# Kernel optimization log

Hardware: AMD Instinct MI355X
Metric: run time of the kernel (lower is better)

The kernel has to match this reference:

```python
import jax, jax.numpy as jnp
import numpy as np
from jax import lax

S, D_IN, D_FC, H_LSTM, H_RNN, D_OUT = 16384, 6, 20, 48, 24, 2


def _lstm_layer(seq, Wih, Whh, bih, bhh):
    # seq: [S, d_in]; PyTorch gate order: i, f, g, o
    H = Whh.shape[1]
    xW = seq @ Wih.T + (bih + bhh)  # [S, 4H] precomputed input projections

    def step(carry, xw):
        h, c = carry
        g = xw + h @ Whh.T
        i = jax.nn.sigmoid(g[:H])
        f = jax.nn.sigmoid(g[H:2 * H])
        gg = jnp.tanh(g[2 * H:3 * H])
        o = jax.nn.sigmoid(g[3 * H:])
        c = f * c + i * gg
        h = o * jnp.tanh(c)
        return (h, c), h

    z = jnp.zeros((H,), seq.dtype)
    _, hs = lax.scan(step, (z, z), xW)
    return hs  # [S, H]


def _rnn_layer(seq, Wih, Whh, bih, bhh):
    H = Whh.shape[1]
    xW = seq @ Wih.T + (bih + bhh)

    def step(h, xw):
        h = jnp.tanh(xw + h @ Whh.T)
        return h, h

    _, hs = lax.scan(step, jnp.zeros((H,), seq.dtype), xW)
    return hs


def setup_inputs() -> dict:
    key = jax.random.key(0)
    ks = iter(jax.random.split(key, 32))

    def p(shape, fan_in):
        s = 1.0 / np.sqrt(fan_in)
        return jax.random.uniform(next(ks), shape, jnp.float32, -s, s)

    inp = {"x": jax.random.normal(next(ks), (S, D_IN), jnp.float32)}
    inp["fc1_W"] = p((D_FC, D_IN), D_IN)
    inp["fc1_b"] = p((D_FC,), D_IN)
    inp["fc2_W"] = p((D_FC, D_FC), D_FC)
    inp["fc2_b"] = p((D_FC,), D_FC)
    # LSTM layer 0: input 20 -> hidden 48
    inp["lstm0_Wih"] = p((4 * H_LSTM, D_FC), H_LSTM)
    inp["lstm0_Whh"] = p((4 * H_LSTM, H_LSTM), H_LSTM)
    inp["lstm0_bih"] = p((4 * H_LSTM,), H_LSTM)
    inp["lstm0_bhh"] = p((4 * H_LSTM,), H_LSTM)
    # LSTM layers 1..4: input 48 -> hidden 48, stacked
    inp["lstmr_Wih"] = p((4, 4 * H_LSTM, H_LSTM), H_LSTM)
    inp["lstmr_Whh"] = p((4, 4 * H_LSTM, H_LSTM), H_LSTM)
    inp["lstmr_bih"] = p((4, 4 * H_LSTM), H_LSTM)
    inp["lstmr_bhh"] = p((4, 4 * H_LSTM), H_LSTM)
    # RNN layer 0: 48 -> 24, layer 1: 24 -> 24
    inp["rnn0_Wih"] = p((H_RNN, H_LSTM), H_RNN)
    inp["rnn0_Whh"] = p((H_RNN, H_RNN), H_RNN)
    inp["rnn0_bih"] = p((H_RNN,), H_RNN)
    inp["rnn0_bhh"] = p((H_RNN,), H_RNN)
    inp["rnn1_Wih"] = p((H_RNN, H_RNN), H_RNN)
    inp["rnn1_Whh"] = p((H_RNN, H_RNN), H_RNN)
    inp["rnn1_bih"] = p((H_RNN,), H_RNN)
    inp["rnn1_bhh"] = p((H_RNN,), H_RNN)
    inp["fc4_W"] = p((D_OUT, H_RNN), H_RNN)
    inp["fc4_b"] = p((D_OUT,), H_RNN)
    return inp


def reference(x, fc1_W, fc1_b, fc2_W, fc2_b,
              lstm0_Wih, lstm0_Whh, lstm0_bih, lstm0_bhh,
              lstmr_Wih, lstmr_Whh, lstmr_bih, lstmr_bhh,
              rnn0_Wih, rnn0_Whh, rnn0_bih, rnn0_bhh,
              rnn1_Wih, rnn1_Whh, rnn1_bih, rnn1_bhh,
              fc4_W, fc4_b):
    h = jax.nn.relu(x @ fc1_W.T + fc1_b)
    h = jax.nn.relu(h @ fc2_W.T + fc2_b)
    h = _lstm_layer(h, lstm0_Wih, lstm0_Whh, lstm0_bih, lstm0_bhh)
    for l in range(4):  # fixed small layer loop
        h = _lstm_layer(h, lstmr_Wih[l], lstmr_Whh[l], lstmr_bih[l], lstmr_bhh[l])
    h = _rnn_layer(h, rnn0_Wih, rnn0_Whh, rnn0_bih, rnn0_bhh)
    h = _rnn_layer(h, rnn1_Wih, rnn1_Whh, rnn1_bih, rnn1_bhh)
    h = jax.nn.relu(h)
    out = h @ fc4_W.T + fc4_b  # [S, 2]
    return out[None]  # [1, S, 2] matching batch_first torch output
```

## Files before the change

kernel.cpp:

```cpp
#include <hip/hip_runtime.h>
#include <hip/hip_bf16.h>

#define S_LEN 16384
#define N_IN 23
#define CH2 32
#define NCH2 (S_LEN / CH2)
#define RING_D 8

typedef float v2f __attribute__((ext_vector_type(2)));
typedef _Float16 h2v __attribute__((ext_vector_type(2)));

__device__ __forceinline__ float fsig(float x) {
    return __builtin_amdgcn_rcpf(1.f + __expf(-x));
}
__device__ __forceinline__ float ftanh_fast(float x) {
    float e = __expf(-2.f * fabsf(x));
    float r = (1.f - e) * __builtin_amdgcn_rcpf(1.f + e);
    return x >= 0.f ? r : -r;
}
__device__ __forceinline__ float rlane(float v, int k) {
    return __uint_as_float(__builtin_amdgcn_readlane(__float_as_uint(v), k));
}
__device__ __forceinline__ h2v rlane_h2(h2v v, int k) {
    int b;
    __builtin_memcpy(&b, &v, 4);
    b = __builtin_amdgcn_readlane(b, k);
    h2v r;
    __builtin_memcpy(&r, &b, 4);
    return r;
}
__device__ __forceinline__ h2v pack_h2(float a, float b) {
    auto p = __builtin_amdgcn_cvt_pkrtz(a, b);
    h2v r;
    __builtin_memcpy(&r, &p, 4);
    return r;
}

#if __has_builtin(__builtin_amdgcn_fdot2)
__device__ __forceinline__ float fdot2_hw(h2v w, h2v h, float acc) {
    return __builtin_amdgcn_fdot2(w, h, acc, false);
}
#define FDOT2(w, h, acc) fdot2_hw((w), (h), (acc))
#else
__device__ __forceinline__ float fdot2_sw(h2v w, h2v h, float acc) {
    return acc + (float)w.x * (float)h.x + (float)w.y * (float)h.y;
}
#define FDOT2(w, h, acc) fdot2_sw((w), (h), (acc))
#endif

__global__ void detect_kernel(const void* probe, int nsamp, int* flag)
{
    if (blockIdx.x == 0 && threadIdx.x == 0) {
        const unsigned short* p = (const unsigned short*)probe;
        int isbf16 = 1;
        for (int i = 0; i < nsamp; i++) {
            float v = __uint_as_float(((unsigned int)p[i]) << 16);
            if (!(fabsf(v) < 1e4f)) { isbf16 = 0; break; }
        }
        *flag = isbf16;
    }
}

struct IngestArgs {
    const void* src[N_IN];
    float*      dst[N_IN];
    int         n[N_IN];
};

__global__ void ingest_kernel(IngestArgs args, const int* __restrict__ flag)
{
    const int isbf16 = *flag;
    const int tid    = blockIdx.x * blockDim.x + threadIdx.x;
    const int stride = gridDim.x * blockDim.x;
    for (int i = 0; i < N_IN; i++) {
        const int n = args.n[i];
        float* dst  = args.dst[i];
        if (isbf16) {
            const unsigned short* s = (const unsigned short*)args.src[i];
            for (int j = tid; j < n; j += stride)
                dst[j] = __uint_as_float(((unsigned int)s[j]) << 16);
        } else {
            const float* s = (const float*)args.src[i];
            for (int j = tid; j < n; j += stride)
                dst[j] = s[j];
        }
    }
}

__global__ void init_kernel(int* prog)
{
    int t = threadIdx.x;
    if (t < 1024) prog[t] = 0;
}

__global__ void fc12_kernel(const float* __restrict__ x,
                            const float* __restrict__ W1, const float* __restrict__ b1,
                            const float* __restrict__ W2, const float* __restrict__ b2,
                            float* __restrict__ h2out)
{
    int s = blockIdx.x * blockDim.x + threadIdx.x;
    if (s >= S_LEN) return;
    float xin[6];
#pragma unroll
    for (int k = 0; k < 6; k++) xin[k] = x[s * 6 + k];
    float h1[20];
#pragma unroll
    for (int j = 0; j < 20; j++) {
        float a = b1[j];
#pragma unroll
        for (int k = 0; k < 6; k++) a += W1[j * 6 + k] * xin[k];
        h1[j] = a > 0.f ? a : 0.f;
    }
#pragma unroll
    for (int j = 0; j < 20; j++) {
        float a = b2[j];
#pragma unroll
        for (int k = 0; k < 20; k++) a += W2[j * 20 + k] * h1[k];
        h2out[s * 20 + j] = a > 0.f ? a : 0.f;
    }
}

template <int DIN, int NG, bool TRANS>
__device__ void producer_block(const float* __restrict__ in,
                               const float* __restrict__ Wih,
                               const float* __restrict__ bih,
                               const float* __restrict__ bhh,
                               float* __restrict__ ring,
                               int* my_prog, int* in_prog, int* cons_prog,
                               float* smem)
{
    constexpr int GR  = NG / 3;
    constexpr int GS  = 256 / GR;
    constexpr int SLT = CH2 / GS;

    const int t  = threadIdx.x;
    const int rg = t % GR;
    const int sg = t / GR;

    float* in_sh = smem;
    float* xw_sh = smem + CH2 * DIN;

    float w[3][DIN];
    float bs[3];
    int cellr[3], partr[3];
#pragma unroll
    for (int r = 0; r < 3; r++) {
        const int row = rg * 3 + r;
#pragma unroll
        for (int k = 0; k < DIN; k++) w[r][k] = Wih[row * DIN + k];
        bs[r] = bih[row] + bhh[row];
        cellr[r] = row % 48;
        partr[r] = row / 48;
    }

    const float4* x4 = (const float4*)in_sh;

    for (int c = 0; c < NCH2; c++) {
        if (t == 0) {
            if (in_prog) {
                while (__hip_atomic_load(in_prog, __ATOMIC_ACQUIRE, __HIP_MEMORY_SCOPE_AGENT) < c + 1)
                    __builtin_amdgcn_s_sleep(1);
            }
            if (c >= RING_D) {
                while (__hip_atomic_load(cons_prog, __ATOMIC_ACQUIRE, __HIP_MEMORY_SCOPE_AGENT) < c - RING_D + 1)
                    __builtin_amdgcn_s_sleep(1);
            }
        }
        __syncthreads();
        {
            const float4* gsrc = (const float4*)(in + (size_t)c * CH2 * DIN);
            float4* ldst = (float4*)in_sh;
            for (int i = t; i < CH2 * DIN / 4; i += 256) ldst[i] = gsrc[i];
        }
        __syncthreads();

#pragma unroll
        for (int i = 0; i < SLT; i++) {
            const int sl = sg * SLT + i;
            float a0 = bs[0], a1 = bs[1], a2 = bs[2];
#pragma unroll
            for (int k = 0; k < DIN / 4; k++) {
                float4 xv = x4[sl * (DIN / 4) + k];
                a0 += w[0][4 * k + 0] * xv.x; a0 += w[0][4 * k + 1] * xv.y;
                a0 += w[0][4 * k + 2] * xv.z; a0 += w[0][4 * k + 3] * xv.w;
                a1 += w[1][4 * k + 0] * xv.x; a1 += w[1][4 * k + 1] * xv.y;
                a1 += w[1][4 * k + 2] * xv.z; a1 += w[1][4 * k + 3] * xv.w;
                a2 += w[2][4 * k + 0] * xv.x; a2 += w[2][4 * k + 1] * xv.y;
                a2 += w[2][4 * k + 2] * xv.z; a2 += w[2][4 * k + 3] * xv.w;
            }
            if (TRANS) {
                xw_sh[(sl * 48 + cellr[0]) * 4 + partr[0]] = a0;
                xw_sh[(sl * 48 + cellr[1]) * 4 + partr[1]] = a1;
                xw_sh[(sl * 48 + cellr[2]) * 4 + partr[2]] = a2;
            } else {
                xw_sh[sl * NG + rg * 3 + 0] = a0;
                xw_sh[sl * NG + rg * 3 + 1] = a1;
                xw_sh[sl * NG + rg * 3 + 2] = a2;
            }
        }
        __syncthreads();
        {
            const float4* lsrc = (const float4*)xw_sh;
            float4* gdst = (float4*)(ring + (size_t)(c % RING_D) * CH2 * NG);
            for (int i = t; i < CH2 * NG / 4; i += 256) gdst[i] = lsrc[i];
        }
        __syncthreads();
        if (t == 0)
            __hip_atomic_store(my_prog, c + 1, __ATOMIC_RELEASE, __HIP_MEMORY_SCOPE_AGENT);
    }
}

__device__ void lstm_scan(const float* __restrict__ Whh,
                          const float* __restrict__ ring,
                          float* __restrict__ hseq,
                          int* my_prog, int* prod_prog, float* smem)
{
    const int t = threadIdx.x;
    const int j = (t < 48) ? t : 47;
    float* xw_buf = smem;
    float* hh_buf = smem + 12288;

    h2v wI[24], wF[24], wG[24], wO[24];
    if (t < 64) {
#pragma unroll
        for (int k = 0; k < 24; k++) {
            wI[k] = pack_h2(Whh[j * 48 + 2 * k],         Whh[j * 48 + 2 * k + 1]);
            wF[k] = pack_h2(Whh[(48 + j) * 48 + 2 * k],  Whh[(48 + j) * 48 + 2 * k + 1]);
            wG[k] = pack_h2(Whh[(96 + j) * 48 + 2 * k],  Whh[(96 + j) * 48 + 2 * k + 1]);
            wO[k] = pack_h2(Whh[(144 + j) * 48 + 2 * k], Whh[(144 + j) * 48 + 2 * k + 1]);
        }
    }
    float hvec = 0.f, ccell = 0.f;

    if (t >= 128) {
        while (__hip_atomic_load(prod_prog, __ATOMIC_ACQUIRE, __HIP_MEMORY_SCOPE_AGENT) < 1)
            __builtin_amdgcn_s_sleep(8);
        const float4* g = (const float4*)ring;
        float4* d = (float4*)xw_buf;
        for (int i = t - 128; i < CH2 * 48; i += 128) d[i] = g[i];
    }
    __syncthreads();

    for (int c = 0; c < NCH2; c++) {
        if (t < 64) {
            const float4* xf = (const float4*)(xw_buf + (c & 1) * (CH2 * 192));
            float* hh = hh_buf + (c & 1) * (CH2 * 48);
            float4 xw4 = xf[j];
            for (int sl = 0; sl < CH2; sl++) {
                float4 nxt = xf[(sl + 1 < CH2 ? sl + 1 : sl) * 48 + j];
                float hn = __shfl_down(hvec, 1, 64);
                h2v hp = pack_h2(hvec, hn);
                float aI0 = xw4.x, aF0 = xw4.y, aG0 = xw4.z, aO0 = xw4.w;
                float aI1 = 0.f, aF1 = 0.f, aG1 = 0.f, aO1 = 0.f;
#pragma unroll
                for (int kp = 0; kp < 12; kp++) {
                    h2v hb = rlane_h2(hp, 2 * kp);
                    aI0 = FDOT2(wI[kp], hb, aI0);
                    aF0 = FDOT2(wF[kp], hb, aF0);
                    aG0 = FDOT2(wG[kp], hb, aG0);
                    aO0 = FDOT2(wO[kp], hb, aO0);
                }
#pragma unroll
                for (int kp = 12; kp < 24; kp++) {
                    h2v hb = rlane_h2(hp, 2 * kp);
                    aI1 = FDOT2(wI[kp], hb, aI1);
                    aF1 = FDOT2(wF[kp], hb, aF1);
                    aG1 = FDOT2(wG[kp], hb, aG1);
                    aO1 = FDOT2(wO[kp], hb, aO1);
                }
                float iv = fsig(aI0 + aI1);
                float fv = fsig(aF0 + aF1);
                float gv = 2.f * fsig(2.f * (aG0 + aG1)) - 1.f;
                float ov = fsig(aO0 + aO1);
                ccell = fv * ccell + iv * gv;
                float h = ov * ftanh_fast(ccell);
                hvec = h;
                if (t < 48) hh[sl * 48 + t] = h;
                xw4 = nxt;
            }
        } else if (t < 128) {
            if (c >= 1) {
                const float4* s4 = (const float4*)(hh_buf + ((c - 1) & 1) * (CH2 * 48));
                float4* d4 = (float4*)(hseq + (size_t)(c - 1) * CH2 * 48);
                for (int i = t - 64; i < CH2 * 12; i += 64) d4[i] = s4[i];
                if (t == 64)
                    __hip_atomic_store(my_prog, c, __ATOMIC_RELEASE, __HIP_MEMORY_SCOPE_AGENT);
            }
        } else {
            if (c + 1 < NCH2) {
                while (__hip_atomic_load(prod_prog, __ATOMIC_ACQUIRE, __HIP_MEMORY_SCOPE_AGENT) < c + 2)
                    __builtin_amdgcn_s_sleep(8);
                const float4* g = (const float4*)(ring + (size_t)((c + 1) % RING_D) * CH2 * 192);
                float4* d = (float4*)(xw_buf + ((c + 1) & 1) * (CH2 * 192));
                for (int i = t - 128; i < CH2 * 48; i += 128) d[i] = g[i];
            }
        }
        __syncthreads();
    }
    if (t >= 64 && t < 128) {
        const float4* s4 = (const float4*)(hh_buf + ((NCH2 - 1) & 1) * (CH2 * 48));
        float4* d4 = (float4*)(hseq + (size_t)(NCH2 - 1) * CH2 * 48);
        for (int i = t - 64; i < CH2 * 12; i += 64) d4[i] = s4[i];
        if (t == 64)
            __hip_atomic_store(my_prog, NCH2, __ATOMIC_RELEASE, __HIP_MEMORY_SCOPE_AGENT);
    }
}

__device__ void rnn_scan(const float* __restrict__ Whh,
                         const float* __restrict__ ring,
                         float* __restrict__ hseq,
                         int* my_prog, int* prod_prog, float* smem)
{
    const int t = threadIdx.x;
    float* xw_buf = smem;
    float* hh_buf = smem + 1536;

    float whh[24];
    if (t < 24) {
#pragma unroll
        for (int k = 0; k < 24; k++) whh[k] = Whh[t * 24 + k];
    }
    float hvec = 0.f;

    if (t >= 128) {
        while (__hip_atomic_load(prod_prog, __ATOMIC_ACQUIRE, __HIP_MEMORY_SCOPE_AGENT) < 1)
            __builtin_amdgcn_s_sleep(8);
        const float4* g = (const float4*)ring;
        float4* d = (float4*)xw_buf;
        for (int i = t - 128; i < CH2 * 6; i += 128) d[i] = g[i];
    }
    __syncthreads();

    for (int c = 0; c < NCH2; c++) {
        if (t < 64) {
            const float* xwc = xw_buf + (c & 1) * (CH2 * 24);
            float* hh = hh_buf + (c & 1) * (CH2 * 24);
            float xwv = (t < 24) ? xwc[t] : 0.f;
            for (int sl = 0; sl < CH2; sl++) {
                float nxtx = (t < 24) ? xwc[((sl + 1 < CH2) ? sl + 1 : sl) * 24 + t] : 0.f;
                float a0 = xwv, a1 = 0.f, a2 = 0.f, a3 = 0.f;
#pragma unroll
                for (int k = 0; k < 24; k += 4) {
                    a0 += rlane(hvec, k + 0) * whh[k + 0];
                    a1 += rlane(hvec, k + 1) * whh[k + 1];
                    a2 += rlane(hvec, k + 2) * whh[k + 2];
                    a3 += rlane(hvec, k + 3) * whh[k + 3];
                }
                float h = ftanh_fast((a0 + a1) + (a2 + a3));
                if (t < 24) {
                    hvec = h;
                    hh[sl * 24 + t] = h;
                }
                xwv = nxtx;
            }
        } else if (t < 128) {
            if (c >= 1) {
                const float4* s4 = (const float4*)(hh_buf + ((c - 1) & 1) * (CH2 * 24));
                float4* d4 = (float4*)(hseq + (size_t)(c - 1) * CH2 * 24);
                for (int i = t - 64; i < CH2 * 6; i += 64) d4[i] = s4[i];
                if (t == 64)
                    __hip_atomic_store(my_prog, c, __ATOMIC_RELEASE, __HIP_MEMORY_SCOPE_AGENT);
            }
        } else {
            if (c + 1 < NCH2) {
                while (__hip_atomic_load(prod_prog, __ATOMIC_ACQUIRE, __HIP_MEMORY_SCOPE_AGENT) < c + 2)
                    __builtin_amdgcn_s_sleep(8);
                const float4* g = (const float4*)(ring + (size_t)((c + 1) % RING_D) * CH2 * 24);
                float4* d = (float4*)(xw_buf + ((c + 1) & 1) * (CH2 * 24));
                for (int i = t - 128; i < CH2 * 6; i += 128) d[i] = g[i];
            }
        }
        __syncthreads();
    }
    if (t >= 64 && t < 128) {
        const float4* s4 = (const float4*)(hh_buf + ((NCH2 - 1) & 1) * (CH2 * 24));
        float4* d4 = (float4*)(hseq + (size_t)(NCH2 - 1) * CH2 * 24);
        for (int i = t - 64; i < CH2 * 6; i += 64) d4[i] = s4[i];
        if (t == 64)
            __hip_atomic_store(my_prog, NCH2, __ATOMIC_RELEASE, __HIP_MEMORY_SCOPE_AGENT);
    }
}

struct PipeArgs {
    const float* h2;
    const float* l0_Wih; const float* l0_Whh; const float* l0_bih; const float* l0_bhh;
    const float* lr_Wih; const float* lr_Whh; const float* lr_bih; const float* lr_bhh;
    const float* r0_Wih; const float* r0_Whh; const float* r0_bih; const float* r0_bhh;
    const float* r1_Wih; const float* r1_Whh; const float* r1_bih; const float* r1_bhh;
    float* seq0; float* seq1; float* seq2; float* seq3; float* seq4;
    float* rnnA; float* rnnB;
    float* ring[7];
    int* prog;
};

__global__ void __launch_bounds__(256, 1) pipeline_kernel(PipeArgs a)
{
    __shared__ __align__(16) float smem[15360];
    const int b = blockIdx.x;
    const float* seqin[7] = {a.h2, a.seq0, a.seq1, a.seq2, a.seq3, a.seq4, a.rnnA};
    float* seqout[7] = {a.seq0, a.seq1, a.seq2, a.seq3, a.seq4, a.rnnA, a.rnnB};
    int* sp[7]; int* pp[7];
    for (int l = 0; l < 7; l++) { sp[l] = a.prog + l * 64; pp[l] = a.prog + (8 + l) * 64; }

    if (b < 7) {
        const int l = b;
        int* inp = (l == 0) ? nullptr : sp[l - 1];
        if (l == 0) {
            producer_block<20, 192, true>(a.h2, a.l0_Wih, a.l0_bih, a.l0_bhh,
                                          a.ring[0], pp[0], inp, sp[0], smem);
        } else if (l <= 4) {
            producer_block<48, 192, true>(seqin[l],
                                          a.lr_Wih + (size_t)(l - 1) * 192 * 48,
                                          a.lr_bih + (size_t)(l - 1) * 192,
                                          a.lr_bhh + (size_t)(l - 1) * 192,
                                          a.ring[l], pp[l], inp, sp[l], smem);
        } else if (l == 5) {
            producer_block<48, 24, false>(a.seq4, a.r0_Wih, a.r0_bih, a.r0_bhh,
                                          a.ring[5], pp[5], inp, sp[5], smem);
        } else {
            producer_block<24, 24, false>(a.rnnA, a.r1_Wih, a.r1_bih, a.r1_bhh,
                                          a.ring[6], pp[6], inp, sp[6], smem);
        }
    } else {
        const int l = b - 7;
        if (l == 0) {
            lstm_scan(a.l0_Whh, a.ring[0], seqout[0], sp[0], pp[0], smem);
        } else if (l <= 4) {
            lstm_scan(a.lr_Whh + (size_t)(l - 1) * 192 * 48,
                      a.ring[l], seqout[l], sp[l], pp[l], smem);
        } else if (l == 5) {
            rnn_scan(a.r0_Whh, a.ring[5], seqout[5], sp[5], pp[5], smem);
        } else {
            rnn_scan(a.r1_Whh, a.ring[6], seqout[6], sp[6], pp[6], smem);
        }
    }
}

__global__ void out_kernel(const float* __restrict__ hin,
                           const float* __restrict__ W,
                           const float* __restrict__ b,
                           void* __restrict__ out,
                           const int* __restrict__ flag)
{
    int s = blockIdx.x * blockDim.x + threadIdx.x;
    if (s >= S_LEN) return;
    const int isbf16 = *flag;
    float h[24];
#pragma unroll
    for (int k = 0; k < 24; k++) {
        float v = hin[s * 24 + k];
        h[k] = v > 0.f ? v : 0.f;
    }
#pragma unroll
    for (int j = 0; j < 2; j++) {
        float a = b[j];
#pragma unroll
        for (int k = 0; k < 24; k++) a += W[j * 24 + k] * h[k];
        if (isbf16) ((__hip_bfloat16*)out)[s * 2 + j] = __float2bfloat16(a);
        else        ((float*)out)[s * 2 + j] = a;
    }
}

extern "C" void kernel_launch(void* const* d_in, const int* in_sizes, int n_in,
                              void* d_out, int out_size, void* d_ws, size_t ws_size,
                              hipStream_t stream)
{
    int*   ip    = (int*)d_ws;
    int*   flag  = ip;
    int*   prog  = ip + 256;
    float* ws    = (float*)d_ws;
    float* conv0 = ws + 4096;

    IngestArgs ia;
    float* conv[N_IN];
    {
        float* p = conv0;
        for (int i = 0; i < N_IN; i++) {
            conv[i] = p;
            ia.src[i] = d_in[i];
            ia.dst[i] = p;
            ia.n[i]   = in_sizes[i];
            p += in_sizes[i];
        }
    }
    float* h2   = conv0 + 191000;
    float* seq0 = h2 + 327680;
    float* seq1 = seq0 + 786432;
    float* seq2 = seq1 + 786432;
    float* seq3 = seq2 + 786432;
    float* seq4 = seq3 + 786432;
    float* rnnA = seq4 + 786432;
    float* rnnB = rnnA + 393216;
    float* rbase = rnnB + 393216;
    float* ring[7];
    {
        float* p = rbase;
        for (int l = 0; l < 5; l++) { ring[l] = p; p += RING_D * CH2 * 192; }
        for (int l = 5; l < 7; l++) { ring[l] = p; p += RING_D * CH2 * 24;  }
    }

    const int TPB = 256;
    const int NB  = S_LEN / TPB;

    detect_kernel<<<1, 64, 0, stream>>>(d_in[1], in_sizes[1], flag);
    ingest_kernel<<<128, 256, 0, stream>>>(ia, flag);
    init_kernel<<<1, 1024, 0, stream>>>(prog);

    fc12_kernel<<<NB, TPB, 0, stream>>>(conv[0], conv[1], conv[2], conv[3], conv[4], h2);

    PipeArgs pa;
    pa.h2 = h2;
    pa.l0_Wih = conv[5];  pa.l0_Whh = conv[6];  pa.l0_bih = conv[7];  pa.l0_bhh = conv[8];
    pa.lr_Wih = conv[9];  pa.lr_Whh = conv[10]; pa.lr_bih = conv[11]; pa.lr_bhh = conv[12];
    pa.r0_Wih = conv[13]; pa.r0_Whh = conv[14]; pa.r0_bih = conv[15]; pa.r0_bhh = conv[16];
    pa.r1_Wih = conv[17]; pa.r1_Whh = conv[18]; pa.r1_bih = conv[19]; pa.r1_bhh = conv[20];
    pa.seq0 = seq0; pa.seq1 = seq1; pa.seq2 = seq2; pa.seq3 = seq3; pa.seq4 = seq4;
    pa.rnnA = rnnA; pa.rnnB = rnnB;
    for (int l = 0; l < 7; l++) pa.ring[l] = ring[l];
    pa.prog = prog;

    pipeline_kernel<<<14, 256, 0, stream>>>(pa);

    out_kernel<<<NB, TPB, 0, stream>>>(rnnB, conv[21], conv[22], d_out, flag);
}
```

Baseline: 6.070 ms.

## Use fp32 FMA recurrence with log2e-prescaled weights and per-role wave barriers

Replaces the packed fp16 dot2 recurrence in the LSTM scan with plain fp32 FMAs over 48 readlane broadcasts. Weights and biases are prescaled by log2(e), or 2·log2(e) for the g gate, so the gates can use raw exp2. The gate maths is merged to share reciprocals: one rcp covers the i·g product and one covers o·tanh(c). The per-chunk loop is also split into separate role branches that synchronise with an explicit s_barrier, which cuts branch overhead on the critical wave. This doubles the FMA count and the weight register footprint (192 fp32 registers), trading those for fewer conversions, fewer transcendental ops and better precision.

```diff
diff --git a/kernel.cpp b/kernel.cpp
--- a/kernel.cpp
+++ b/kernel.cpp
@@ -7,11 +7,15 @@
 #define NCH2 (S_LEN / CH2)
 #define RING_D 8
 
-typedef float v2f __attribute__((ext_vector_type(2)));
-typedef _Float16 h2v __attribute__((ext_vector_type(2)));
-
-__device__ __forceinline__ float fsig(float x) {
-    return __builtin_amdgcn_rcpf(1.f + __expf(-x));
+#define L2E     1.442695041f
+#define TWO_L2E 2.885390082f
+
+__device__ __forceinline__ float fexp2(float x) {
+#if __has_builtin(__builtin_amdgcn_exp2f)
+    return __builtin_amdgcn_exp2f(x);
+#else
+    return exp2f(x);
+#endif
 }
 __device__ __forceinline__ float ftanh_fast(float x) {
     float e = __expf(-2.f * fabsf(x));
@@ -21,32 +25,11 @@
 __device__ __forceinline__ float rlane(float v, int k) {
     return __uint_as_float(__builtin_amdgcn_readlane(__float_as_uint(v), k));
 }
-__device__ __forceinline__ h2v rlane_h2(h2v v, int k) {
-    int b;
-    __builtin_memcpy(&b, &v, 4);
-    b = __builtin_amdgcn_readlane(b, k);
-    h2v r;
-    __builtin_memcpy(&r, &b, 4);
-    return r;
-}
-__device__ __forceinline__ h2v pack_h2(float a, float b) {
-    auto p = __builtin_amdgcn_cvt_pkrtz(a, b);
-    h2v r;
-    __builtin_memcpy(&r, &p, 4);
-    return r;
-}
-
-#if __has_builtin(__builtin_amdgcn_fdot2)
-__device__ __forceinline__ float fdot2_hw(h2v w, h2v h, float acc) {
-    return __builtin_amdgcn_fdot2(w, h, acc, false);
-}
-#define FDOT2(w, h, acc) fdot2_hw((w), (h), (acc))
-#else
-__device__ __forceinline__ float fdot2_sw(h2v w, h2v h, float acc) {
-    return acc + (float)w.x * (float)h.x + (float)w.y * (float)h.y;
-}
-#define FDOT2(w, h, acc) fdot2_sw((w), (h), (acc))
-#endif
+
+__device__ __forceinline__ void wave_bar() {
+    asm volatile("s_waitcnt vmcnt(0) lgkmcnt(0)" ::: "memory");
+    __builtin_amdgcn_s_barrier();
+}
 
 __global__ void detect_kernel(const void* probe, int nsamp, int* flag)
 {
@@ -146,9 +129,10 @@
 #pragma unroll
     for (int r = 0; r < 3; r++) {
         const int row = rg * 3 + r;
-#pragma unroll
-        for (int k = 0; k < DIN; k++) w[r][k] = Wih[row * DIN + k];
-        bs[r] = bih[row] + bhh[row];
+        const float fac = TRANS ? ((row / 48) == 2 ? TWO_L2E : L2E) : 1.f;
+#pragma unroll
+        for (int k = 0; k < DIN; k++) w[r][k] = Wih[row * DIN + k] * fac;
+        bs[r] = (bih[row] + bhh[row]) * fac;
         cellr[r] = row % 48;
         partr[r] = row / 48;
     }
@@ -216,69 +200,57 @@
                           int* my_prog, int* prod_prog, float* smem)
 {
     const int t = threadIdx.x;
-    const int j = (t < 48) ? t : 47;
     float* xw_buf = smem;
     float* hh_buf = smem + 12288;
 
-    h2v wI[24], wF[24], wG[24], wO[24];
     if (t < 64) {
-#pragma unroll
-        for (int k = 0; k < 24; k++) {
-            wI[k] = pack_h2(Whh[j * 48 + 2 * k],         Whh[j * 48 + 2 * k + 1]);
-            wF[k] = pack_h2(Whh[(48 + j) * 48 + 2 * k],  Whh[(48 + j) * 48 + 2 * k + 1]);
-            wG[k] = pack_h2(Whh[(96 + j) * 48 + 2 * k],  Whh[(96 + j) * 48 + 2 * k + 1]);
-            wO[k] = pack_h2(Whh[(144 + j) * 48 + 2 * k], Whh[(144 + j) * 48 + 2 * k + 1]);
-        }
-    }
-    float hvec = 0.f, ccell = 0.f;
-
-    if (t >= 128) {
-        while (__hip_atomic_load(prod_prog, __ATOMIC_ACQUIRE, __HIP_MEMORY_SCOPE_AGENT) < 1)
-            __builtin_amdgcn_s_sleep(8);
-        const float4* g = (const float4*)ring;
-        float4* d = (float4*)xw_buf;
-        for (int i = t - 128; i < CH2 * 48; i += 128) d[i] = g[i];
-    }
-    __syncthreads();
-
-    for (int c = 0; c < NCH2; c++) {
-        if (t < 64) {
-            const float4* xf = (const float4*)(xw_buf + (c & 1) * (CH2 * 192));
+        const int j = (t < 48) ? t : 47;
+        float wi[48], wf[48], wg[48], wo[48];
+#pragma unroll
+        for (int k = 0; k < 48; k++) {
+            wi[k] = Whh[j * 48 + k] * L2E;
+            wf[k] = Whh[(48 + j) * 48 + k] * L2E;
+            wg[k] = Whh[(96 + j) * 48 + k] * TWO_L2E;
+            wo[k] = Whh[(144 + j) * 48 + k] * L2E;
+        }
+        float hvec = 0.f, ccell = 0.f;
+        wave_bar();
+
+        for (int c = 0; c < NCH2; c++) {
+            const float4* xf = (const float4*)(xw_buf + (c & 1) * (CH2 * 192)) + j;
             float* hh = hh_buf + (c & 1) * (CH2 * 48);
-            float4 xw4 = xf[j];
+            float4 xw4 = xf[0];
             for (int sl = 0; sl < CH2; sl++) {
-                float4 nxt = xf[(sl + 1 < CH2 ? sl + 1 : sl) * 48 + j];
-                float hn = __shfl_down(hvec, 1, 64);
-                h2v hp = pack_h2(hvec, hn);
-                float aI0 = xw4.x, aF0 = xw4.y, aG0 = xw4.z, aO0 = xw4.w;
-                float aI1 = 0.f, aF1 = 0.f, aG1 = 0.f, aO1 = 0.f;
-#pragma unroll
-                for (int kp = 0; kp < 12; kp++) {
-                    h2v hb = rlane_h2(hp, 2 * kp);
-                    aI0 = FDOT2(wI[kp], hb, aI0);
-                    aF0 = FDOT2(wF[kp], hb, aF0);
-                    aG0 = FDOT2(wG[kp], hb, aG0);
-                    aO0 = FDOT2(wO[kp], hb, aO0);
+                float4 nxt = xf[(sl + 1) * 48];
+                float aI = xw4.x, aF = xw4.y, aG = xw4.z, aO = xw4.w;
+#pragma unroll
+                for (int k = 0; k < 48; k++) {
+                    float hk = rlane(hvec, k);
+                    aI = fmaf(hk, wi[k], aI);
+                    aF = fmaf(hk, wf[k], aF);
+                    aG = fmaf(hk, wg[k], aG);
+                    aO = fmaf(hk, wo[k], aO);
                 }
-#pragma unroll
-                for (int kp = 12; kp < 24; kp++) {
-                    h2v hb = rlane_h2(hp, 2 * kp);
-                    aI1 = FDOT2(wI[kp], hb, aI1);
-                    aF1 = FDOT2(wF[kp], hb, aF1);
-                    aG1 = FDOT2(wG[kp], hb, aG1);
-                    aO1 = FDOT2(wO[kp], hb, aO1);
-                }
-                float iv = fsig(aI0 + aI1);
-                float fv = fsig(aF0 + aF1);
-                float gv = 2.f * fsig(2.f * (aG0 + aG1)) - 1.f;
-                float ov = fsig(aO0 + aO1);
-                ccell = fv * ccell + iv * gv;
-                float h = ov * ftanh_fast(ccell);
+                float eI = fexp2(-aI);
+                float eF = fexp2(-aF);
+                float eG = fexp2(-fabsf(aG));
+                float eO = fexp2(-aO);
+                float fv = __builtin_amdgcn_rcpf(1.f + eF);
+                float ig = (1.f - eG) * __builtin_amdgcn_rcpf((1.f + eI) * (1.f + eG));
+                ig = __int_as_float(__float_as_int(ig) ^ (__float_as_int(aG) & 0x80000000));
+                ccell = fmaf(fv, ccell, ig);
+                float eC = fexp2(-TWO_L2E * fabsf(ccell));
+                float r  = (1.f - eC) * __builtin_amdgcn_rcpf((1.f + eO) * (1.f + eC));
+                float h  = __int_as_float(__float_as_int(r) ^ (__float_as_int(ccell) & 0x80000000));
                 hvec = h;
                 if (t < 48) hh[sl * 48 + t] = h;
                 xw4 = nxt;
             }
-        } else if (t < 128) {
+            wave_bar();
+        }
+    } else if (t < 128) {
+        wave_bar();
+        for (int c = 0; c < NCH2; c++) {
             if (c >= 1) {
                 const float4* s4 = (const float4*)(hh_buf + ((c - 1) & 1) * (CH2 * 48));
                 float4* d4 = (float4*)(hseq + (size_t)(c - 1) * CH2 * 48);
@@ -286,7 +258,25 @@
                 if (t == 64)
                     __hip_atomic_store(my_prog, c, __ATOMIC_RELEASE, __HIP_MEMORY_SCOPE_AGENT);
             }
-        } else {
+            wave_bar();
+        }
+        {
+            const float4* s4 = (const float4*)(hh_buf + ((NCH2 - 1) & 1) * (CH2 * 48));
+            float4* d4 = (float4*)(hseq + (size_t)(NCH2 - 1) * CH2 * 48);
+            for (int i = t - 64; i < CH2 * 12; i += 64) d4[i] = s4[i];
+            if (t == 64)
+                __hip_atomic_store(my_prog, NCH2, __ATOMIC_RELEASE, __HIP_MEMORY_SCOPE_AGENT);
+        }
+    } else {
+        while (__hip_atomic_load(prod_prog, __ATOMIC_ACQUIRE, __HIP_MEMORY_SCOPE_AGENT) < 1)
+            __builtin_amdgcn_s_sleep(8);
+        {
+            const float4* g = (const float4*)ring;
+            float4* d = (float4*)xw_buf;
+            for (int i = t - 128; i < CH2 * 48; i += 128) d[i] = g[i];
+        }
+        wave_bar();
+        for (int c = 0; c < NCH2; c++) {
             if (c + 1 < NCH2) {
                 while (__hip_atomic_load(prod_prog, __ATOMIC_ACQUIRE, __HIP_MEMORY_SCOPE_AGENT) < c + 2)
                     __builtin_amdgcn_s_sleep(8);
@@ -294,15 +284,8 @@
                 float4* d = (float4*)(xw_buf + ((c + 1) & 1) * (CH2 * 192));
                 for (int i = t - 128; i < CH2 * 48; i += 128) d[i] = g[i];
             }
-        }
-        __syncthreads();
-    }
-    if (t >= 64 && t < 128) {
-        const float4* s4 = (const float4*)(hh_buf + ((NCH2 - 1) & 1) * (CH2 * 48));
-        float4* d4 = (float4*)(hseq + (size_t)(NCH2 - 1) * CH2 * 48);
-        for (int i = t - 64; i < CH2 * 12; i += 64) d4[i] = s4[i];
-        if (t == 64)
-            __hip_atomic_store(my_prog, NCH2, __ATOMIC_RELEASE, __HIP_MEMORY_SCOPE_AGENT);
+            wave_bar();
+        }
     }
 }
 
```

New measurement: 11.00 ms. +81.2%, slower.
